# Kernel optimization log

Measured on AMD Instinct MI355X. Metric: run time of the kernel, lower is better.

## Reference

```python
import jax, jax.numpy as jnp
import numpy as np

D_MODEL = 1024
N_HEAD = 16
ATT_DIM = D_MODEL // N_HEAD


def setup_inputs() -> dict:
    key = jax.random.key(0)
    ks = jax.random.split(key, 7)
    B, S = 2, 2048
    q = jax.random.normal(ks[0], (B, S, D_MODEL), dtype=jnp.float32)
    k = jax.random.normal(ks[1], (B, S, D_MODEL), dtype=jnp.float32)
    v = jax.random.normal(ks[2], (B, S, D_MODEL), dtype=jnp.float32)
    # per-head projection weights, stored as [H, d_model, att_dim] (x @ W form)
    scale_qkv = float(np.sqrt(6.0 / (D_MODEL + ATT_DIM)))  # xavier_uniform
    Wq = jax.random.uniform(ks[3], (N_HEAD, D_MODEL, ATT_DIM), jnp.float32, -scale_qkv, scale_qkv)
    Wk = jax.random.uniform(ks[4], (N_HEAD, D_MODEL, ATT_DIM), jnp.float32, -scale_qkv, scale_qkv)
    Wv = jax.random.uniform(ks[5], (N_HEAD, D_MODEL, ATT_DIM), jnp.float32, -scale_qkv, scale_qkv)
    scale_o = float(np.sqrt(6.0 / (D_MODEL + D_MODEL)))
    Wo = jax.random.uniform(ks[6], (D_MODEL, D_MODEL), jnp.float32, -scale_o, scale_o)
    return {"q": q, "k": k, "v": v, "Wq": Wq, "Wk": Wk, "Wv": Wv, "Wo": Wo}


def reference(q, k, v, Wq, Wk, Wv, Wo):
    # per-head projections, batched over heads: [H,B,S,E]
    qh = jnp.einsum('bsd,hde->hbse', q, Wq)
    kh = jnp.einsum('bsd,hde->hbse', k, Wk)
    vh = jnp.einsum('bsd,hde->hbse', v, Wv)
    # NOTE: original divides by att_dim (not sqrt(att_dim))
    scores = jnp.einsum('hbqe,hbke->hbqk', qh, kh) / ATT_DIM
    attn = jax.nn.softmax(scores, axis=-1)  # [H,B,Sq,Sk]
    att = jnp.einsum('hbqk,hbke->hbqe', attn, vh)  # [H,B,S,E]
    # concat heads along last dim in head order, then output projection
    H, B, S, E = att.shape
    cat = jnp.transpose(att, (1, 2, 0, 3)).reshape(B, S, H * E)
    out = cat @ Wo  # dropout is identity in eval
    return (out, attn)
```

## Files before the change

kernel.cpp:

```cpp
#include <hip/hip_runtime.h>
#include <hip/hip_bf16.h>

#define DM 1024
#define NH 16
#define AD 64
#define BB 2
#define SS 2048
#define LOG2E 1.44269504f

typedef float f32x4 __attribute__((ext_vector_type(4)));
typedef short bf16x8 __attribute__((ext_vector_type(8)));
typedef unsigned short u16;
typedef unsigned int u32;
typedef u16 u16x4 __attribute__((ext_vector_type(4)));
typedef u16 u16x8 __attribute__((ext_vector_type(8)));
typedef u32 u32x4 __attribute__((ext_vector_type(4)));

static __device__ __forceinline__ u16 f2bf(float f) {
  unsigned u = __builtin_bit_cast(unsigned, f);
  u += 0x7fffu + ((u >> 16) & 1u);
  return (u16)(u >> 16);
}

#define MFMA16(a, b, c) __builtin_amdgcn_mfma_f32_16x16x32_bf16((a), (b), (c), 0, 0, 0)

static __device__ __forceinline__ void ld_lds16(const void* g, void* l) {
  __builtin_amdgcn_global_load_lds((const __attribute__((address_space(1))) u32*)g,
                                   (__attribute__((address_space(3))) u32*)l, 16, 0, 0);
}

#define WAITV(N)                                             \
  do {                                                       \
    asm volatile("s_waitcnt vmcnt(" #N ")" ::: "memory");    \
    __builtin_amdgcn_sched_barrier(0);                       \
  } while (0)
#define WAITL0()                                             \
  do {                                                       \
    asm volatile("s_waitcnt lgkmcnt(0)" ::: "memory");       \
    __builtin_amdgcn_sched_barrier(0);                       \
  } while (0)
#define BAR() __builtin_amdgcn_s_barrier()

#define KFRAG(buf, row, P) (*(const bf16x8*)(&(buf)[(row) * 64 + ((((P) ^ ((row) & 7))) << 3)]))
#define V64(buf, row, P, hh) \
  (*(const u16x4*)(&(buf)[(row) * 64 + ((((P) ^ ((row) & 7))) << 3) + (hh) * 4]))

__global__ __launch_bounds__(256, 4) void cast3_kernel(const float* __restrict__ s0,
                                                       const float* __restrict__ s1,
                                                       const float* __restrict__ s2,
                                                       u16* __restrict__ d0, u16* __restrict__ d1,
                                                       u16* __restrict__ d2, int n8) {
  const float* src = blockIdx.y == 0 ? s0 : blockIdx.y == 1 ? s1 : s2;
  u16* dst = blockIdx.y == 0 ? d0 : blockIdx.y == 1 ? d1 : d2;
  int i = blockIdx.x * blockDim.x + threadIdx.x;
  int stride = gridDim.x * blockDim.x;
  for (; i < n8; i += stride) {
    const f32x4* p = (const f32x4*)src + 2 * (size_t)i;
    f32x4 a = p[0], b = p[1];
    u16x8 o;
    o[0] = f2bf(a[0]); o[1] = f2bf(a[1]); o[2] = f2bf(a[2]); o[3] = f2bf(a[3]);
    o[4] = f2bf(b[0]); o[5] = f2bf(b[1]); o[6] = f2bf(b[2]); o[7] = f2bf(b[3]);
    *((u16x8*)dst + i) = o;
  }
}

template <int MODE>
__global__ __launch_bounds__(256, 4) void tcast_kernel(const float* __restrict__ s0,
                                                       const float* __restrict__ s1,
                                                       const float* __restrict__ s2,
                                                       u16* __restrict__ dst, int R, int C,
                                                       float scale0) {
  __shared__ float T[64][65];
  const float* src;
  u16* dstp;
  float scale;
  long bo;
  if (MODE == 0) {
    src = s0; bo = (long)blockIdx.z * R * C; dstp = dst; scale = scale0;
  } else {
    int which = blockIdx.z >> 4, zz = blockIdx.z & 15;
    src = which == 0 ? s0 : which == 1 ? s1 : s2;
    bo = (long)zz * R * C;
    dstp = dst + (long)which * NH * R * C;
    scale = which == 0 ? scale0 : 1.0f;
  }
  int r0 = blockIdx.x * 64, c0 = blockIdx.y * 64;
  int cl = threadIdx.x & 63, rl = threadIdx.x >> 6;
#pragma unroll
  for (int i = 0; i < 16; i++) {
    int rr = rl + 4 * i;
    T[cl][rr] = src[bo + (long)(r0 + rr) * C + c0 + cl];
  }
  __syncthreads();
#pragma unroll
  for (int i = 0; i < 16; i++) {
    int cc = rl + 4 * i;
    dstp[bo + (long)(c0 + cc) * R + r0 + cl] = f2bf(T[cc][cl] * scale);
  }
}

template <int MODE>
__global__ __launch_bounds__(256, 5) void proj_kernel(const u16* __restrict__ X,
                                                      const u16* __restrict__ WT,
                                                      void* __restrict__ outp, long ob, long oh,
                                                      long os, long oe) {
  __shared__ u16 Ab[2][64 * 64];
  __shared__ u16 Bb[2][64 * 64];
  int s0 = blockIdx.x * 64, h = blockIdx.y, b = blockIdx.z;
  int tid = threadIdx.x, w = tid >> 6, lane = tid & 63, g = lane >> 4, li = lane & 15;
  const u16* xb = X + ((long)b * SS + s0) * DM;
  const u16* wb = WT + (long)h * 64 * DM;
  int r1 = tid >> 3, p1 = (tid ^ (r1 & 7)) & 7;
  int r2 = (tid + 256) >> 3, p2 = ((tid + 256) ^ (r2 & 7)) & 7;
  const u16* as1 = xb + (long)r1 * DM + p1 * 8;
  const u16* as2 = xb + (long)r2 * DM + p2 * 8;
  const u16* bs1 = wb + (long)r1 * DM + p1 * 8;
  const u16* bs2 = wb + (long)r2 * DM + p2 * 8;
  u16* ad0 = &Ab[0][tid * 8]; u16* ad0b = &Ab[0][(tid + 256) * 8];
  u16* ad1 = &Ab[1][tid * 8]; u16* ad1b = &Ab[1][(tid + 256) * 8];
  u16* bd0 = &Bb[0][tid * 8]; u16* bd0b = &Bb[0][(tid + 256) * 8];
  u16* bd1 = &Bb[1][tid * 8]; u16* bd1b = &Bb[1][(tid + 256) * 8];

  ld_lds16(as1, ad0); ld_lds16(as2, ad0b);
  ld_lds16(bs1, bd0); ld_lds16(bs2, bd0b);

  f32x4 acc[4] = {};
  for (int kc = 0; kc < DM / 64; kc++) {
    if (kc + 1 < DM / 64) {
      int ko = (kc + 1) * 64;
      if (kc & 1) {
        ld_lds16(as1 + ko, ad0); ld_lds16(as2 + ko, ad0b);
        ld_lds16(bs1 + ko, bd0); ld_lds16(bs2 + ko, bd0b);
      } else {
        ld_lds16(as1 + ko, ad1); ld_lds16(as2 + ko, ad1b);
        ld_lds16(bs1 + ko, bd1); ld_lds16(bs2 + ko, bd1b);
      }
      WAITV(4);
    } else {
      WAITV(0);
    }
    BAR();
    const u16* ab = Ab[kc & 1];
    const u16* bbuf = Bb[kc & 1];
    bf16x8 bf0 = KFRAG(bbuf, w * 16 + li, g);
    bf16x8 bf1 = KFRAG(bbuf, w * 16 + li, 4 + g);
#pragma unroll
    for (int mi = 0; mi < 4; mi++) {
      bf16x8 a0 = KFRAG(ab, mi * 16 + li, g);
      bf16x8 a1 = KFRAG(ab, mi * 16 + li, 4 + g);
      acc[mi] = MFMA16(a0, bf0, acc[mi]);
      acc[mi] = MFMA16(a1, bf1, acc[mi]);
    }
    WAITL0();
    BAR();
  }

  int e = w * 16 + li;
  long bh = (long)b * ob + (long)h * oh;
#pragma unroll
  for (int mi = 0; mi < 4; mi++) {
    int sb = s0 + mi * 16 + 4 * g;
    if (MODE == 0) {
      u16* o = (u16*)outp;
#pragma unroll
      for (int r = 0; r < 4; r++) o[bh + (long)(sb + r) * os + (long)e * oe] = f2bf(acc[mi][r]);
    } else if (MODE == 1) {
      u16x4 v;
#pragma unroll
      for (int r = 0; r < 4; r++) v[r] = f2bf(acc[mi][r]);
      *(u16x4*)((u16*)outp + bh + (long)e * oe + sb) = v;
    } else {
      float* o = (float*)outp;
#pragma unroll
      for (int r = 0; r < 4; r++) o[bh + (long)(sb + r) * os + (long)e * oe] = acc[mi][r];
    }
  }
}

__global__ __launch_bounds__(512, 4) void attn_kernel(const u16* __restrict__ qh,
                                                      const u16* __restrict__ kh,
                                                      const u16* __restrict__ vhT,
                                                      float* __restrict__ attn_out,
                                                      u16* __restrict__ cat) {
  __shared__ u16 Kb[2][64 * 64];
  __shared__ u16 Vb[2][64 * 64];
  int h = blockIdx.y, b = blockIdx.z;
  int hb = h * BB + b;
  int tid = threadIdx.x;
  int w = tid >> 6, lane = tid & 63;
  int g = lane >> 4, li = lane & 15;
  long base = (long)hb * SS * AD;
  const u16* qhb = qh + base;
  const u16* khb = kh + base;
  const u16* vhb = vhT + base;
  int q0 = blockIdx.x * 128 + w * 16;

  bf16x8 bq0 = *(const bf16x8*)(qhb + (q0 + li) * AD + 8 * g);
  bf16x8 bq1 = *(const bf16x8*)(qhb + (q0 + li) * AD + 32 + 8 * g);

  int srow = tid >> 3, spiece = (tid ^ (srow & 7)) & 7;
  const u16* ksrc = khb + (long)srow * AD + spiece * 8;
  const u16* vsrc = vhb + (long)srow * SS + spiece * 8;
  u16* kd0 = &Kb[0][tid * 8]; u16* kd1 = &Kb[1][tid * 8];
  u16* vd0 = &Vb[0][tid * 8]; u16* vd1 = &Vb[1][tid * 8];

  float m_run = -3.0e38f, l_run = 0.f;
  ld_lds16(ksrc, kd0);
  for (int ch = 0; ch < SS / 64; ch++) {
    if (ch + 1 < SS / 64) {
      ld_lds16(ksrc + (ch + 1) * 64 * AD, (ch & 1) ? kd0 : kd1);
      WAITV(1);
    } else {
      WAITV(0);
    }
    BAR();
    const u16* kb = Kb[ch & 1];
    f32x4 sacc[4] = {};
#pragma unroll
    for (int mi = 0; mi < 4; mi++) {
      bf16x8 a0 = KFRAG(kb, mi * 16 + li, g);
      bf16x8 a1 = KFRAG(kb, mi * 16 + li, 4 + g);
      sacc[mi] = MFMA16(a0, bq0, sacc[mi]);
      sacc[mi] = MFMA16(a1, bq1, sacc[mi]);
    }
    float cm = m_run;
#pragma unroll
    for (int c = 0; c < 4; c++)
#pragma unroll
      for (int r = 0; r < 4; r++) cm = fmaxf(cm, sacc[c][r]);
    l_run *= exp2f((m_run - cm) * LOG2E);
#pragma unroll
    for (int c = 0; c < 4; c++)
#pragma unroll
      for (int r = 0; r < 4; r++) l_run += exp2f((sacc[c][r] - cm) * LOG2E);
    m_run = cm;
    WAITL0();
    BAR();
  }
#pragma unroll
  for (int d = 16; d <= 32; d <<= 1) {
    float om = __shfl_xor(m_run, d);
    float ol = __shfl_xor(l_run, d);
    float nm = fmaxf(m_run, om);
    l_run = l_run * exp2f((m_run - nm) * LOG2E) + ol * exp2f((om - nm) * LOG2E);
    m_run = nm;
  }
  float moff = m_run * LOG2E + log2f(l_run);

  ld_lds16(ksrc, kd0);
  ld_lds16(vsrc, vd0);
  f32x4 accv[4] = {};
  float* arow = attn_out + ((long)hb * SS + q0 + li) * SS;
  for (int ch = 0; ch < SS / 64; ch++) {
    if (ch + 1 < SS / 64) {
      ld_lds16(ksrc + (ch + 1) * 64 * AD, (ch & 1) ? kd0 : kd1);
      ld_lds16(vsrc + (ch + 1) * 64, (ch & 1) ? vd0 : vd1);
      if (ch == 0) {
        WAITV(2);
      } else {
        WAITV(6);
      }
    } else {
      WAITV(4);
    }
    BAR();
    const u16* kb = Kb[ch & 1];
    const u16* vb = Vb[ch & 1];
    f32x4 sacc[4] = {};
#pragma unroll
    for (int mi = 0; mi < 4; mi++) {
      bf16x8 a0 = KFRAG(kb, mi * 16 + li, g);
      bf16x8 a1 = KFRAG(kb, mi * 16 + li, 4 + g);
      sacc[mi] = MFMA16(a0, bq0, sacc[mi]);
      sacc[mi] = MFMA16(a1, bq1, sacc[mi]);
    }
    u32 pw[8];
#pragma unroll
    for (int c = 0; c < 4; c++) {
      f32x4 pv;
#pragma unroll
      for (int r = 0; r < 4; r++) pv[r] = exp2f(sacc[c][r] * LOG2E - moff);
      *(f32x4*)(arow + ch * 64 + c * 16 + 4 * g) = pv;
      pw[2 * c] = (u32)f2bf(pv[0]) | ((u32)f2bf(pv[1]) << 16);
      pw[2 * c + 1] = (u32)f2bf(pv[2]) | ((u32)f2bf(pv[3]) << 16);
    }
#pragma unroll
    for (int kk = 0; kk < 2; kk++) {
      u32x4 aw = {pw[4 * kk], pw[4 * kk + 1], pw[4 * kk + 2], pw[4 * kk + 3]};
      bf16x8 ap = __builtin_bit_cast(bf16x8, aw);
#pragma unroll
      for (int et = 0; et < 4; et++) {
        int row = et * 16 + li;
        u16x4 b0 = V64(vb, row, 4 * kk + (g >> 1), g & 1);
        u16x4 b1 = V64(vb, row, 4 * kk + 2 + (g >> 1), g & 1);
        u16x8 ub = {b0[0], b0[1], b0[2], b0[3], b1[0], b1[1], b1[2], b1[3]};
        bf16x8 bv = __builtin_bit_cast(bf16x8, ub);
        accv[et] = MFMA16(ap, bv, accv[et]);
      }
    }
    WAITL0();
    BAR();
  }

#pragma unroll
  for (int et = 0; et < 4; et++)
#pragma unroll
    for (int r = 0; r < 4; r++)
      cat[((long)b * SS + q0 + 4 * g + r) * DM + h * AD + et * 16 + li] = f2bf(accv[et][r]);
}

extern "C" void kernel_launch(void* const* d_in, const int* in_sizes, int n_in, void* d_out,
                              int out_size, void* d_ws, size_t ws_size, hipStream_t stream) {
  const float* q = (const float*)d_in[0];
  const float* k = (const float*)d_in[1];
  const float* v = (const float*)d_in[2];
  const float* Wq = (const float*)d_in[3];
  const float* Wk = (const float*)d_in[4];
  const float* Wv = (const float*)d_in[5];
  const float* Wo = (const float*)d_in[6];
  float* out = (float*)d_out;
  float* attn_out = out + (long)BB * SS * DM;

  const long NX = (long)BB * SS * DM;
  const long NW = (long)NH * DM * AD;
  u16* ws = (u16*)d_ws;
  u16* xq = ws;
  u16* xk = xq + NX;
  u16* xv = xk + NX;
  u16* WqT = xv + NX;
  u16* WkT = WqT + NW;
  u16* WvT = WkT + NW;
  u16* WoT = WvT + NW;
  u16* qhw = WoT + (long)DM * DM;
  u16* khw = qhw + NX;
  u16* vhw = khw + NX;
  u16* catw = vhw + NX;

  cast3_kernel<<<dim3(700, 3), 256, 0, stream>>>(q, k, v, xq, xk, xv, (int)(NX / 8));
  tcast_kernel<1><<<dim3(16, 1, 48), 256, 0, stream>>>(Wq, Wk, Wv, WqT, DM, AD, 1.0f / AD);
  tcast_kernel<0><<<dim3(16, 16, 1), 256, 0, stream>>>(Wo, nullptr, nullptr, WoT, DM, DM, 1.0f);

  dim3 pg(SS / 64, NH, BB);
  proj_kernel<0><<<pg, 256, 0, stream>>>(xq, WqT, qhw, (long)SS * AD, (long)BB * SS * AD, AD, 1);
  proj_kernel<0><<<pg, 256, 0, stream>>>(xk, WkT, khw, (long)SS * AD, (long)BB * SS * AD, AD, 1);
  proj_kernel<1><<<pg, 256, 0, stream>>>(xv, WvT, vhw, (long)SS * AD, (long)BB * SS * AD, 1, SS);

  attn_kernel<<<dim3(SS / 128, NH, BB), 512, 0, stream>>>(qhw, khw, vhw, attn_out, catw);

  proj_kernel<2><<<pg, 256, 0, stream>>>(catw, WoT, out, (long)SS * DM, AD, DM, 1);
}
```

Baseline: 282.0 us.

## Read K/V straight from global memory and drop running-max softmax tracking

The attention kernel stops staging K and V tiles in LDS with async loads and barriers. Each wave now reads its K and V fragments directly from global memory, relying on L1/L2 for reuse across the 4 waves. The first pass keeps only a running sum of exp2 with no running max. The log2(e) factor is folded into the Wq cast scale, and the block shrinks from 512 to 256 threads. This removes barrier, LDS and max/rescale overhead, but it adds redundant global traffic, and exponentials can overflow if scores are ever large.

```diff
diff --git a/kernel.cpp b/kernel.cpp
--- a/kernel.cpp
+++ b/kernel.cpp
@@ -42,8 +42,6 @@
 #define BAR() __builtin_amdgcn_s_barrier()
 
 #define KFRAG(buf, row, P) (*(const bf16x8*)(&(buf)[(row) * 64 + ((((P) ^ ((row) & 7))) << 3)]))
-#define V64(buf, row, P, hh) \
-  (*(const u16x4*)(&(buf)[(row) * 64 + ((((P) ^ ((row) & 7))) << 3) + (hh) * 4]))
 
 __global__ __launch_bounds__(256, 4) void cast3_kernel(const float* __restrict__ s0,
                                                        const float* __restrict__ s1,
@@ -177,100 +175,54 @@
   }
 }
 
-__global__ __launch_bounds__(512, 4) void attn_kernel(const u16* __restrict__ qh,
+__global__ __launch_bounds__(256, 4) void attn_kernel(const u16* __restrict__ qh,
                                                       const u16* __restrict__ kh,
                                                       const u16* __restrict__ vhT,
                                                       float* __restrict__ attn_out,
                                                       u16* __restrict__ cat) {
-  __shared__ u16 Kb[2][64 * 64];
-  __shared__ u16 Vb[2][64 * 64];
   int h = blockIdx.y, b = blockIdx.z;
   int hb = h * BB + b;
   int tid = threadIdx.x;
-  int w = tid >> 6, lane = tid & 63;
+  int wv = tid >> 6, lane = tid & 63;
   int g = lane >> 4, li = lane & 15;
   long base = (long)hb * SS * AD;
   const u16* qhb = qh + base;
   const u16* khb = kh + base;
   const u16* vhb = vhT + base;
-  int q0 = blockIdx.x * 128 + w * 16;
+  int q0 = (blockIdx.x * 4 + wv) * 16;
 
   bf16x8 bq0 = *(const bf16x8*)(qhb + (q0 + li) * AD + 8 * g);
   bf16x8 bq1 = *(const bf16x8*)(qhb + (q0 + li) * AD + 32 + 8 * g);
 
-  int srow = tid >> 3, spiece = (tid ^ (srow & 7)) & 7;
-  const u16* ksrc = khb + (long)srow * AD + spiece * 8;
-  const u16* vsrc = vhb + (long)srow * SS + spiece * 8;
-  u16* kd0 = &Kb[0][tid * 8]; u16* kd1 = &Kb[1][tid * 8];
-  u16* vd0 = &Vb[0][tid * 8]; u16* vd1 = &Vb[1][tid * 8];
-
-  float m_run = -3.0e38f, l_run = 0.f;
-  ld_lds16(ksrc, kd0);
+  float l_run = 0.f;
   for (int ch = 0; ch < SS / 64; ch++) {
-    if (ch + 1 < SS / 64) {
-      ld_lds16(ksrc + (ch + 1) * 64 * AD, (ch & 1) ? kd0 : kd1);
-      WAITV(1);
-    } else {
-      WAITV(0);
-    }
-    BAR();
-    const u16* kb = Kb[ch & 1];
     f32x4 sacc[4] = {};
 #pragma unroll
     for (int mi = 0; mi < 4; mi++) {
-      bf16x8 a0 = KFRAG(kb, mi * 16 + li, g);
-      bf16x8 a1 = KFRAG(kb, mi * 16 + li, 4 + g);
+      long krow = ch * 64 + mi * 16 + li;
+      bf16x8 a0 = *(const bf16x8*)(khb + krow * AD + 8 * g);
+      bf16x8 a1 = *(const bf16x8*)(khb + krow * AD + 32 + 8 * g);
       sacc[mi] = MFMA16(a0, bq0, sacc[mi]);
       sacc[mi] = MFMA16(a1, bq1, sacc[mi]);
     }
-    float cm = m_run;
 #pragma unroll
     for (int c = 0; c < 4; c++)
 #pragma unroll
-      for (int r = 0; r < 4; r++) cm = fmaxf(cm, sacc[c][r]);
-    l_run *= exp2f((m_run - cm) * LOG2E);
-#pragma unroll
-    for (int c = 0; c < 4; c++)
-#pragma unroll
-      for (int r = 0; r < 4; r++) l_run += exp2f((sacc[c][r] - cm) * LOG2E);
-    m_run = cm;
-    WAITL0();
-    BAR();
-  }
-#pragma unroll
-  for (int d = 16; d <= 32; d <<= 1) {
-    float om = __shfl_xor(m_run, d);
-    float ol = __shfl_xor(l_run, d);
-    float nm = fmaxf(m_run, om);
-    l_run = l_run * exp2f((m_run - nm) * LOG2E) + ol * exp2f((om - nm) * LOG2E);
-    m_run = nm;
-  }
-  float moff = m_run * LOG2E + log2f(l_run);
-
-  ld_lds16(ksrc, kd0);
-  ld_lds16(vsrc, vd0);
+      for (int r = 0; r < 4; r++) l_run += exp2f(sacc[c][r]);
+  }
+  l_run += __shfl_xor(l_run, 16);
+  l_run += __shfl_xor(l_run, 32);
+  float moff = log2f(l_run);
+
   f32x4 accv[4] = {};
   float* arow = attn_out + ((long)hb * SS + q0 + li) * SS;
   for (int ch = 0; ch < SS / 64; ch++) {
-    if (ch + 1 < SS / 64) {
-      ld_lds16(ksrc + (ch + 1) * 64 * AD, (ch & 1) ? kd0 : kd1);
-      ld_lds16(vsrc + (ch + 1) * 64, (ch & 1) ? vd0 : vd1);
-      if (ch == 0) {
-        WAITV(2);
-      } else {
-        WAITV(6);
-      }
-    } else {
-      WAITV(4);
-    }
-    BAR();
-    const u16* kb = Kb[ch & 1];
-    const u16* vb = Vb[ch & 1];
     f32x4 sacc[4] = {};
 #pragma unroll
     for (int mi = 0; mi < 4; mi++) {
-      bf16x8 a0 = KFRAG(kb, mi * 16 + li, g);
-      bf16x8 a1 = KFRAG(kb, mi * 16 + li, 4 + g);
+      long krow = ch * 64 + mi * 16 + li;
+      bf16x8 a0 = *(const bf16x8*)(khb + krow * AD + 8 * g);
+      bf16x8 a1 = *(const bf16x8*)(khb + krow * AD + 32 + 8 * g);
       sacc[mi] = MFMA16(a0, bq0, sacc[mi]);
       sacc[mi] = MFMA16(a1, bq1, sacc[mi]);
     }
@@ -279,7 +231,7 @@
     for (int c = 0; c < 4; c++) {
       f32x4 pv;
 #pragma unroll
-      for (int r = 0; r < 4; r++) pv[r] = exp2f(sacc[c][r] * LOG2E - moff);
+      for (int r = 0; r < 4; r++) pv[r] = exp2f(sacc[c][r] - moff);
       *(f32x4*)(arow + ch * 64 + c * 16 + 4 * g) = pv;
       pw[2 * c] = (u32)f2bf(pv[0]) | ((u32)f2bf(pv[1]) << 16);
       pw[2 * c + 1] = (u32)f2bf(pv[2]) | ((u32)f2bf(pv[3]) << 16);
@@ -290,16 +242,15 @@
       bf16x8 ap = __builtin_bit_cast(bf16x8, aw);
 #pragma unroll
       for (int et = 0; et < 4; et++) {
-        int row = et * 16 + li;
-        u16x4 b0 = V64(vb, row, 4 * kk + (g >> 1), g & 1);
-        u16x4 b1 = V64(vb, row, 4 * kk + 2 + (g >> 1), g & 1);
+        long row = et * 16 + li;
+        const u16* vrow = vhb + row * SS + ch * 64 + kk * 32 + 4 * g;
+        u16x4 b0 = *(const u16x4*)(vrow);
+        u16x4 b1 = *(const u16x4*)(vrow + 16);
         u16x8 ub = {b0[0], b0[1], b0[2], b0[3], b1[0], b1[1], b1[2], b1[3]};
         bf16x8 bv = __builtin_bit_cast(bf16x8, ub);
         accv[et] = MFMA16(ap, bv, accv[et]);
       }
     }
-    WAITL0();
-    BAR();
   }
 
 #pragma unroll
@@ -337,7 +288,7 @@
   u16* catw = vhw + NX;
 
   cast3_kernel<<<dim3(700, 3), 256, 0, stream>>>(q, k, v, xq, xk, xv, (int)(NX / 8));
-  tcast_kernel<1><<<dim3(16, 1, 48), 256, 0, stream>>>(Wq, Wk, Wv, WqT, DM, AD, 1.0f / AD);
+  tcast_kernel<1><<<dim3(16, 1, 48), 256, 0, stream>>>(Wq, Wk, Wv, WqT, DM, AD, LOG2E / AD);
   tcast_kernel<0><<<dim3(16, 16, 1), 256, 0, stream>>>(Wo, nullptr, nullptr, WoT, DM, DM, 1.0f);
 
   dim3 pg(SS / 64, NH, BB);
@@ -345,7 +296,7 @@
   proj_kernel<0><<<pg, 256, 0, stream>>>(xk, WkT, khw, (long)SS * AD, (long)BB * SS * AD, AD, 1);
   proj_kernel<1><<<pg, 256, 0, stream>>>(xv, WvT, vhw, (long)SS * AD, (long)BB * SS * AD, 1, SS);
 
-  attn_kernel<<<dim3(SS / 128, NH, BB), 512, 0, stream>>>(qhw, khw, vhw, attn_out, catw);
+  attn_kernel<<<dim3(SS / 64, NH, BB), 256, 0, stream>>>(qhw, khw, vhw, attn_out, catw);
 
   proj_kernel<2><<<pg, 256, 0, stream>>>(catw, WoT, out, (long)SS * DM, AD, DM, 1);
 }
```

Result: slower. 580.5 us (+105.8%).
